# Kernel tuning notes

Hardware: AMD Instinct MI355X
Metric: run time of the kernel (lower is better)

Reference implementation:

```python
import jax, jax.numpy as jnp
import numpy as np

K, D = 4096, 256
BETA, DECAY, EPS = 0.25, 0.99, 1e-05
B = 32768


def setup_inputs() -> dict:
    key = jax.random.key(0)
    k1, k2, k3, k4 = jax.random.split(key, 4)
    return {
        "z_e": jax.random.normal(k1, (B, D), dtype=jnp.float32),
        "codebook": jax.random.normal(k2, (K, D), dtype=jnp.float32),
        "ema_cluster_size": jax.random.uniform(k3, (K,), dtype=jnp.float32),
        "ema_weight": jax.random.normal(k4, (K, D), dtype=jnp.float32),
    }


def reference(z_e, codebook, ema_cluster_size, ema_weight):
    z_e = z_e.astype(jnp.float32)
    # squared L2 distances: ||z||^2 - 2 z.C^T + ||C||^2  (chunking in torch is
    # purely a memory optimization; math is identical)
    e_norm = jnp.sum(z_e * z_e, axis=1, keepdims=True)            # [B,1]
    c_norm = jnp.sum(codebook * codebook, axis=1)                  # [K]
    dists = e_norm - 2.0 * (z_e @ codebook.T) + c_norm[None, :]    # [B,K]
    idx = jnp.argmin(dists, axis=1)                                # [B] int

    z_q = codebook[idx]                                            # [B,d] gather

    # EMA codebook update (no_grad in torch)
    counts = jnp.zeros((K,), jnp.float32).at[idx].add(1.0)         # bincount
    new_cluster = ema_cluster_size * DECAY + counts * (1.0 - DECAY)
    dw = jnp.zeros((K, D), jnp.float32).at[idx].add(z_e)           # index_add_
    new_ema_weight = ema_weight * DECAY + dw * (1.0 - DECAY)
    n = jnp.sum(new_cluster)
    cluster_size = (new_cluster + EPS) / (n + K * EPS) * n
    new_codebook = new_ema_weight / cluster_size[:, None]

    z_q_ste = z_e + jax.lax.stop_gradient(z_q - z_e)
    commit = BETA * jnp.mean((z_e - z_q) ** 2)
    return (z_q_ste, idx, commit, new_codebook, new_cluster, new_ema_weight)
```

## Files before the change

### kernel.cpp

```cpp
#include <hip/hip_runtime.h>

#define KC 4096
#define DD 256
#define BB 32768
#define P_BETA 0.25f
#define P_DECAY 0.99f
#define P_EPS 1e-5f
#define TAU 0.5f
#define CHUNK 32

typedef __attribute__((ext_vector_type(8))) short bf16x8;
typedef __attribute__((ext_vector_type(4))) float f32x4;

static __device__ __forceinline__ unsigned short f2bf(float f) {
    unsigned int u = __float_as_uint(f);
    unsigned int r = (u + 0x7fffu + ((u >> 16) & 1u)) >> 16;
    return (unsigned short)r;
}
static __device__ __forceinline__ void gload_lds16(const void* g, void* s) {
    __builtin_amdgcn_global_load_lds(
        (const __attribute__((address_space(1))) unsigned int*)g,
        (__attribute__((address_space(3))) unsigned int*)s, 16, 0, 0);
}

__global__ __launch_bounds__(256) void convert_z_kernel(const float* __restrict__ src,
                                                        unsigned short* __restrict__ dst) {
    int t = blockIdx.x * 256 + threadIdx.x;
    float4 v = ((const float4*)src)[t];
    *(ushort4*)&dst[(size_t)t * 4] =
        make_ushort4(f2bf(v.x), f2bf(v.y), f2bf(v.z), f2bf(v.w));
}

__global__ __launch_bounds__(256) void convert_cb_kernel(const float* __restrict__ cb,
                                                         unsigned short* __restrict__ dst,
                                                         float* __restrict__ cn) {
    int t = blockIdx.x * 256 + threadIdx.x;
    int lane = threadIdx.x & 63;
    int row = blockIdx.x * 4 + (threadIdx.x >> 6);
    float4 v = ((const float4*)cb)[t];
    *(ushort4*)&dst[(size_t)t * 4] =
        make_ushort4(f2bf(v.x), f2bf(v.y), f2bf(v.z), f2bf(v.w));
    float s = v.x * v.x + v.y * v.y + v.z * v.z + v.w * v.w;
#pragma unroll
    for (int m = 32; m; m >>= 1) s += __shfl_xor(s, m);
    if (lane == 0) cn[row] = s;
}

__global__ __launch_bounds__(256, 2) void
mfma_argmin_kernel(const unsigned short* __restrict__ zb,
                   const unsigned short* __restrict__ cbb,
                   const float* __restrict__ cn,
                   float4* __restrict__ cand) {
    __shared__ unsigned short As[128 * 256];
    __shared__ unsigned short Bs[128 * 64];

    const int tid = threadIdx.x;
    const int l = tid & 63, w = tid >> 6;
    const int xcd = blockIdx.x & 7;
    const int half = xcd >> 2;
    const int rb = (blockIdx.x >> 3) * 4 + (xcd & 3);
    const int row0 = rb * 128;
    const int col0 = half * 2048;
    const int wm = w & 1, wn = w >> 1;
    const int m_off = wm * 64, n_off = wn * 64;
    const int lm = l & 15, lq = l >> 4;

    {
        const int lrow = w * 2 + (l >> 5);
        const int coff = ((l & 31) ^ lrow) * 8;
#pragma unroll
        for (int i = 0; i < 16; ++i) {
            gload_lds16(zb + (size_t)(row0 + i * 8 + lrow) * DD + coff,
                        &As[(i * 8 + w * 2) * 256]);
        }
    }

    const int srow = l >> 3;
    const int scol = ((l & 7) ^ srow) * 8;
    const int g0 = w * 4;

    float best[16];
    int bidx[16];
#pragma unroll
    for (int s = 0; s < 16; ++s) { best[s] = 3.4e38f; bidx[s] = 0; }

    for (int kc = 0; kc < 2048; kc += 128) {
        f32x4 acc[4][4];
#pragma unroll
        for (int a = 0; a < 4; ++a)
#pragma unroll
            for (int b = 0; b < 4; ++b) acc[a][b] = (f32x4){0.f, 0.f, 0.f, 0.f};

        for (int dc = 0; dc < 4; ++dc) {
#pragma unroll
            for (int j = 0; j < 4; ++j) {
                const int g = g0 + j;
                const int br = col0 + kc + g * 8 + srow;
                gload_lds16(cbb + (size_t)br * DD + dc * 64 + scol, &Bs[g * 512]);
            }
            __syncthreads();
#pragma unroll
            for (int ks = 0; ks < 2; ++ks) {
                bf16x8 af[4], bfr[4];
                const int cbi = dc * 8 + ks * 4 + lq;
#pragma unroll
                for (int tm = 0; tm < 4; ++tm) {
                    int r = m_off + tm * 16 + lm;
                    af[tm] = *(const bf16x8*)&As[r * 256 + ((cbi ^ (r & 7)) * 8)];
                }
#pragma unroll
                for (int tn = 0; tn < 4; ++tn) {
                    int r = n_off + tn * 16 + lm;
                    bfr[tn] = *(const bf16x8*)&Bs[r * 64 + (((ks * 4 + lq) ^ (r & 7)) * 8)];
                }
#pragma unroll
                for (int tm = 0; tm < 4; ++tm)
#pragma unroll
                    for (int tn = 0; tn < 4; ++tn)
                        acc[tm][tn] = __builtin_amdgcn_mfma_f32_16x16x32_bf16(
                            af[tm], bfr[tn], acc[tm][tn], 0, 0, 0);
            }
            __syncthreads();
        }
#pragma unroll
        for (int tn = 0; tn < 4; ++tn) {
            const int col = col0 + kc + n_off + tn * 16 + lm;
            const float cnv = cn[col];
#pragma unroll
            for (int tm = 0; tm < 4; ++tm)
#pragma unroll
                for (int r = 0; r < 4; ++r) {
                    float dist = fmaf(-2.0f, acc[tm][tn][r], cnv);
                    int s = tm * 4 + r;
                    if (dist < best[s]) { best[s] = dist; bidx[s] = col; }
                }
        }
    }

    float v2[16];
    int i2[16];
#pragma unroll
    for (int s = 0; s < 16; ++s) { v2[s] = 3.4e38f; i2[s] = 0x7fffffff; }
#pragma unroll
    for (int m = 1; m < 16; m <<= 1) {
#pragma unroll
        for (int s = 0; s < 16; ++s) {
            float w1 = __shfl_xor(best[s], m); int j1 = __shfl_xor(bidx[s], m);
            float w2 = __shfl_xor(v2[s], m);   int j2 = __shfl_xor(i2[s], m);
            bool b = (w1 < best[s]) || (w1 == best[s] && j1 < bidx[s]);
            if (b) {
                bool c = (best[s] < w2) || (best[s] == w2 && bidx[s] < j2);
                v2[s] = c ? best[s] : w2; i2[s] = c ? bidx[s] : j2;
                best[s] = w1; bidx[s] = j1;
            } else {
                bool c = (w1 < v2[s]) || (w1 == v2[s] && j1 < i2[s]);
                v2[s] = c ? w1 : v2[s]; i2[s] = c ? j1 : i2[s];
            }
        }
    }

    float4* red = (float4*)As;
    if (lm == 0) {
#pragma unroll
        for (int tm = 0; tm < 4; ++tm)
#pragma unroll
            for (int r = 0; r < 4; ++r) {
                int s = tm * 4 + r;
                int row_local = m_off + tm * 16 + lq * 4 + r;
                red[wn * 128 + row_local] =
                    make_float4(best[s], __int_as_float(bidx[s]), v2[s], __int_as_float(i2[s]));
            }
    }
    __syncthreads();
    if (tid < 128) {
        float4 a = red[tid], b = red[128 + tid];
        float av1 = a.x, av2 = a.z; int ai1 = __float_as_int(a.y), ai2 = __float_as_int(a.w);
        float bv1 = b.x, bv2 = b.z; int bi1 = __float_as_int(b.y), bi2 = __float_as_int(b.w);
        float v1o, v2o; int i1o, i2o;
        bool bb = (bv1 < av1) || (bv1 == av1 && bi1 < ai1);
        if (bb) {
            v1o = bv1; i1o = bi1;
            bool c = (av1 < bv2) || (av1 == bv2 && ai1 < bi2);
            v2o = c ? av1 : bv2; i2o = c ? ai1 : bi2;
        } else {
            v1o = av1; i1o = ai1;
            bool c = (bv1 < av2) || (bv1 == av2 && bi1 < ai2);
            v2o = c ? bv1 : av2; i2o = c ? bi1 : ai2;
        }
        cand[(size_t)half * BB + row0 + tid] =
            make_float4(v1o, __int_as_float(i1o), v2o, __int_as_float(i2o));
    }
}

__global__ __launch_bounds__(256) void merge_kernel(
    const float4* __restrict__ cand, int* __restrict__ idx_i,
    float* __restrict__ idx_f, int4* __restrict__ wl, int* __restrict__ wl_cnt) {
    int i = blockIdx.x * 256 + threadIdx.x;
    float4 a = cand[i], b = cand[(size_t)BB + i];
    float av1 = a.x, av2 = a.z; int ai1 = __float_as_int(a.y), ai2 = __float_as_int(a.w);
    float bv1 = b.x, bv2 = b.z; int bi1 = __float_as_int(b.y), bi2 = __float_as_int(b.w);
    float v1o, v2o; int i1o, i2o;
    bool bb = (bv1 < av1) || (bv1 == av1 && bi1 < ai1);
    if (bb) {
        v1o = bv1; i1o = bi1;
        bool c = (av1 < bv2) || (av1 == bv2 && ai1 < bi2);
        v2o = c ? av1 : bv2; i2o = c ? ai1 : bi2;
    } else {
        v1o = av1; i1o = ai1;
        bool c = (bv1 < av2) || (bv1 == av2 && bi1 < ai2);
        v2o = c ? bv1 : av2; i2o = c ? bi1 : ai2;
    }
    idx_i[i] = i1o;
    idx_f[i] = (float)i1o;
    if (v2o - v1o < TAU) {
        int pos = atomicAdd(wl_cnt, 1);
        wl[pos] = make_int4(i, i1o, i2o, 0);
    }
}

__global__ __launch_bounds__(256) void refine_kernel(
    const int4* __restrict__ wl, const int* __restrict__ wl_cnt,
    const float* __restrict__ z, const float* __restrict__ cb,
    const float* __restrict__ cn, int* __restrict__ idx_i,
    float* __restrict__ idx_f) {
    const int wave = (blockIdx.x * 256 + threadIdx.x) >> 6;
    const int l = threadIdx.x & 63;
    const int n = *wl_cnt;
    for (int it = wave; it < n; it += 1024) {
        int4 e = wl[it];
        int i = e.x, k1 = e.y, k2 = e.z;
        float4 zv = ((const float4*)(z + (size_t)i * DD))[l];
        float4 p = ((const float4*)(cb + (size_t)k1 * DD))[l];
        float4 q = ((const float4*)(cb + (size_t)k2 * DD))[l];
        float s1 = zv.x * p.x + zv.y * p.y + zv.z * p.z + zv.w * p.w;
        float s2 = zv.x * q.x + zv.y * q.y + zv.z * q.z + zv.w * q.w;
#pragma unroll
        for (int m = 32; m; m >>= 1) { s1 += __shfl_xor(s1, m); s2 += __shfl_xor(s2, m); }
        float d1 = cn[k1] - 2.f * s1;
        float d2 = cn[k2] - 2.f * s2;
        int kb = (d2 < d1 || (d2 == d1 && k2 < k1)) ? k2 : k1;
        if (l == 0) { idx_i[i] = kb; idx_f[i] = (float)kb; }
    }
}

__global__ __launch_bounds__(256) void hist_kernel(const int* __restrict__ idx_i,
                                                   int* __restrict__ cnt) {
    int i = blockIdx.x * 256 + threadIdx.x;
    atomicAdd(&cnt[idx_i[i]], 1);
}

__global__ __launch_bounds__(256) void prefix_kernel(const int* __restrict__ cnt,
                                                     int* __restrict__ cursor) {
    __shared__ int ls[257];
    const int t = threadIdx.x;
    int local[16];
    int s = 0;
#pragma unroll
    for (int j = 0; j < 16; ++j) { local[j] = s; s += cnt[t * 16 + j]; }
    ls[t + 1] = s;
    __syncthreads();
    if (t == 0) {
        ls[0] = 0;
        for (int j = 1; j <= 256; ++j) ls[j] += ls[j - 1];
    }
    __syncthreads();
    int off = ls[t];
#pragma unroll
    for (int j = 0; j < 16; ++j) cursor[t * 16 + j] = off + local[j];
}

__global__ __launch_bounds__(256) void scatter_ids_kernel(const int* __restrict__ idx_i,
                                                          int* __restrict__ cursor,
                                                          int* __restrict__ row_of) {
    int i = blockIdx.x * 256 + threadIdx.x;
    int k = idx_i[i];
    int pos = atomicAdd(&cursor[k], 1);
    row_of[pos] = i | (k << 16);
}

__global__ __launch_bounds__(256) void bucket_chunk_kernel(
    const float* __restrict__ z, const int* __restrict__ row_of,
    float* __restrict__ dw) {
    __shared__ int pk[CHUNK];
    const int t = threadIdx.x;
    const int p0 = blockIdx.x * CHUNK;
    if (t < CHUNK) pk[t] = row_of[p0 + t];
    __syncthreads();
    float acc = 0.f;
    int kprev = pk[0] >> 16;
#pragma unroll 4
    for (int j = 0; j < CHUNK; ++j) {
        int p = pk[j];
        int r = p & 0xffff, k = p >> 16;
        if (k != kprev) {
            atomicAdd(&dw[(size_t)kprev * DD + t], acc);
            acc = 0.f;
            kprev = k;
        }
        acc += z[(size_t)r * DD + t];
    }
    atomicAdd(&dw[(size_t)kprev * DD + t], acc);
}

__global__ __launch_bounds__(256) void zq_commit_kernel(const float* __restrict__ z,
                                                        const float* __restrict__ cb,
                                                        const int* __restrict__ idx_i,
                                                        float* __restrict__ zq,
                                                        float* __restrict__ commit_parts) {
    const int w = threadIdx.x >> 6, l = threadIdx.x & 63;
    const int i = blockIdx.x * 4 + w;
    const int k = idx_i[i];
    float4 zv = ((const float4*)z)[(size_t)i * 64 + l];
    float4 cv = ((const float4*)cb)[(size_t)k * 64 + l];
    ((float4*)zq)[(size_t)i * 64 + l] = cv;
    float dx = zv.x - cv.x, dy = zv.y - cv.y, dz = zv.z - cv.z, dq = zv.w - cv.w;
    float s = dx * dx + dy * dy + dz * dz + dq * dq;
#pragma unroll
    for (int m = 32; m; m >>= 1) s += __shfl_xor(s, m);
    __shared__ float ls[4];
    if (l == 0) ls[w] = s;
    __syncthreads();
    if (threadIdx.x == 0) commit_parts[blockIdx.x] = ls[0] + ls[1] + ls[2] + ls[3];
}

__global__ __launch_bounds__(256) void cluster_commit_kernel(
    const float* __restrict__ ema_cs, const int* __restrict__ cnt,
    const float* __restrict__ commit_parts, float* __restrict__ out_cluster,
    float* __restrict__ n_ws, float* __restrict__ out_commit) {
    const int t = threadIdx.x;
    float cs = 0.f;
    for (int j = t; j < BB / 4; j += 256) cs += commit_parts[j];
    float ns = 0.f;
    for (int j = t; j < KC; j += 256) {
        float nc = ema_cs[j] * P_DECAY + (float)cnt[j] * (1.0f - P_DECAY);
        out_cluster[j] = nc;
        ns += nc;
    }
#pragma unroll
    for (int m = 32; m; m >>= 1) { cs += __shfl_xor(cs, m); ns += __shfl_xor(ns, m); }
    __shared__ float lc[4], ln[4];
    if ((t & 63) == 0) { lc[t >> 6] = cs; ln[t >> 6] = ns; }
    __syncthreads();
    if (t == 0) {
        *out_commit = P_BETA * (lc[0] + lc[1] + lc[2] + lc[3]) / (float)((size_t)BB * DD);
        *n_ws = ln[0] + ln[1] + ln[2] + ln[3];
    }
}

__global__ __launch_bounds__(256) void finalize_kernel(const float* __restrict__ ema_w,
                                                       const float* __restrict__ dw,
                                                       const float* __restrict__ out_cluster,
                                                       const float* __restrict__ n_ws,
                                                       float* __restrict__ out_ema_w,
                                                       float* __restrict__ out_codebook) {
    const size_t id = (size_t)blockIdx.x * 256 + threadIdx.x;
    const int k = (int)(id >> 8);
    const float n = *n_ws;
    float nw = ema_w[id] * P_DECAY + dw[id] * (1.0f - P_DECAY);
    out_ema_w[id] = nw;
    float cl = out_cluster[k];
    float csz = (cl + P_EPS) / (n + (float)KC * P_EPS) * n;
    out_codebook[id] = nw / csz;
}

extern "C" void kernel_launch(void* const* d_in, const int* in_sizes, int n_in,
                              void* d_out, int out_size, void* d_ws, size_t ws_size,
                              hipStream_t stream) {
    const float* z      = (const float*)d_in[0];
    const float* cb     = (const float*)d_in[1];
    const float* ema_cs = (const float*)d_in[2];
    const float* ema_w  = (const float*)d_in[3];

    float4* cand = (float4*)d_ws;
    int4* wl = (int4*)(cand + 2 * (size_t)BB);
    unsigned short* zb = (unsigned short*)(wl + BB);
    unsigned short* cbb = zb + (size_t)BB * DD;
    float* dw = (float*)(cbb + (size_t)KC * DD);
    float* c_norm = dw + (size_t)KC * DD;
    int* idx_i = (int*)(c_norm + KC);
    int* cnt = idx_i + BB;
    int* wl_cnt = cnt + KC;
    int* cursor = wl_cnt + 1;
    int* row_of = cursor + KC;
    float* commit_parts = (float*)(row_of + BB);
    float* n_ws = commit_parts + BB / 4;

    float* out        = (float*)d_out;
    float* o_zq       = out;
    float* o_idx      = o_zq + (size_t)BB * DD;
    float* o_commit   = o_idx + BB;
    float* o_codebook = o_commit + 1;
    float* o_cluster  = o_codebook + (size_t)KC * DD;
    float* o_emaw     = o_cluster + KC;

    hipMemsetAsync(cnt, 0, (KC + 1) * sizeof(int), stream);
    hipMemsetAsync(dw, 0, (size_t)KC * DD * sizeof(float), stream);

    convert_z_kernel<<<(BB * DD / 4) / 256, 256, 0, stream>>>(z, zb);
    convert_cb_kernel<<<KC / 4, 256, 0, stream>>>(cb, cbb, c_norm);
    mfma_argmin_kernel<<<(BB / 128) * 2, 256, 0, stream>>>(zb, cbb, c_norm, cand);
    merge_kernel<<<BB / 256, 256, 0, stream>>>(cand, idx_i, o_idx, wl, wl_cnt);
    refine_kernel<<<256, 256, 0, stream>>>(wl, wl_cnt, z, cb, c_norm, idx_i, o_idx);
    hist_kernel<<<BB / 256, 256, 0, stream>>>(idx_i, cnt);
    prefix_kernel<<<1, 256, 0, stream>>>(cnt, cursor);
    scatter_ids_kernel<<<BB / 256, 256, 0, stream>>>(idx_i, cursor, row_of);
    bucket_chunk_kernel<<<BB / CHUNK, 256, 0, stream>>>(z, row_of, dw);
    zq_commit_kernel<<<BB / 4, 256, 0, stream>>>(z, cb, idx_i, o_zq, commit_parts);
    cluster_commit_kernel<<<1, 256, 0, stream>>>(ema_cs, cnt, commit_parts,
                                                 o_cluster, n_ws, o_commit);
    finalize_kernel<<<(KC * DD) / 256, 256, 0, stream>>>(ema_w, dw, o_cluster, n_ws,
                                                         o_emaw, o_codebook);
    (void)in_sizes; (void)n_in; (void)out_size; (void)ws_size;
}
```

Measured before the change: 270.2 us.

## Fuse pipeline kernels to cut launches and memsets

After: 237.9 us. 1.14x faster.

```diff
diff --git a/kernel.cpp b/kernel.cpp
--- a/kernel.cpp
+++ b/kernel.cpp
@@ -23,27 +23,35 @@
         (__attribute__((address_space(3))) unsigned int*)s, 16, 0, 0);
 }
 
-__global__ __launch_bounds__(256) void convert_z_kernel(const float* __restrict__ src,
-                                                        unsigned short* __restrict__ dst) {
-    int t = blockIdx.x * 256 + threadIdx.x;
-    float4 v = ((const float4*)src)[t];
-    *(ushort4*)&dst[(size_t)t * 4] =
-        make_ushort4(f2bf(v.x), f2bf(v.y), f2bf(v.z), f2bf(v.w));
-}
-
-__global__ __launch_bounds__(256) void convert_cb_kernel(const float* __restrict__ cb,
-                                                         unsigned short* __restrict__ dst,
-                                                         float* __restrict__ cn) {
-    int t = blockIdx.x * 256 + threadIdx.x;
-    int lane = threadIdx.x & 63;
-    int row = blockIdx.x * 4 + (threadIdx.x >> 6);
-    float4 v = ((const float4*)cb)[t];
-    *(ushort4*)&dst[(size_t)t * 4] =
-        make_ushort4(f2bf(v.x), f2bf(v.y), f2bf(v.z), f2bf(v.w));
-    float s = v.x * v.x + v.y * v.y + v.z * v.z + v.w * v.w;
-#pragma unroll
-    for (int m = 32; m; m >>= 1) s += __shfl_xor(s, m);
-    if (lane == 0) cn[row] = s;
+#define ZBLK (BB * DD / 4 / 256)
+#define CBLK (KC * DD / 4 / 256)
+__global__ __launch_bounds__(256) void convert_all_kernel(
+    const float* __restrict__ z, const float* __restrict__ cb,
+    unsigned short* __restrict__ zb, unsigned short* __restrict__ cbb,
+    float* __restrict__ cn, int* __restrict__ cnt) {
+    const int b = blockIdx.x;
+    if (b < ZBLK) {
+        int t = b * 256 + threadIdx.x;
+        float4 v = ((const float4*)z)[t];
+        *(ushort4*)&zb[(size_t)t * 4] =
+            make_ushort4(f2bf(v.x), f2bf(v.y), f2bf(v.z), f2bf(v.w));
+    } else if (b < ZBLK + CBLK) {
+        int t = (b - ZBLK) * 256 + threadIdx.x;
+        int lane = threadIdx.x & 63;
+        int row = (b - ZBLK) * 4 + (threadIdx.x >> 6);
+        float4 v = ((const float4*)cb)[t];
+        *(ushort4*)&cbb[(size_t)t * 4] =
+            make_ushort4(f2bf(v.x), f2bf(v.y), f2bf(v.z), f2bf(v.w));
+        float s = v.x * v.x + v.y * v.y + v.z * v.z + v.w * v.w;
+#pragma unroll
+        for (int m = 32; m; m >>= 1) s += __shfl_xor(s, m);
+        if (lane == 0) cn[row] = s;
+    } else {
+        int4* p = (int4*)cnt;
+        int4 zv = make_int4(0, 0, 0, 0);
+#pragma unroll
+        for (int j = 0; j < 4; ++j) p[threadIdx.x * 4 + j] = zv;
+    }
 }
 
 __global__ __launch_bounds__(256, 2) void
@@ -192,10 +200,19 @@
     }
 }
 
-__global__ __launch_bounds__(256) void merge_kernel(
-    const float4* __restrict__ cand, int* __restrict__ idx_i,
-    float* __restrict__ idx_f, int4* __restrict__ wl, int* __restrict__ wl_cnt) {
+__global__ __launch_bounds__(256) void merge_refine_kernel(
+    const float4* __restrict__ cand, const float* __restrict__ z,
+    const float* __restrict__ cb, const float* __restrict__ cn,
+    int* __restrict__ idx_i, float* __restrict__ idx_f,
+    int* __restrict__ cnt, float* __restrict__ dw) {
     int i = blockIdx.x * 256 + threadIdx.x;
+    {
+        float4 zv4 = make_float4(0.f, 0.f, 0.f, 0.f);
+        float4* dp = (float4*)dw;
+        int base = i * 8;
+#pragma unroll
+        for (int j = 0; j < 8; ++j) dp[base + j] = zv4;
+    }
     float4 a = cand[i], b = cand[(size_t)BB + i];
     float av1 = a.x, av2 = a.z; int ai1 = __float_as_int(a.y), ai2 = __float_as_int(a.w);
     float bv1 = b.x, bv2 = b.z; int bi1 = __float_as_int(b.y), bi2 = __float_as_int(b.w);
@@ -210,43 +227,27 @@
         bool c = (bv1 < av2) || (bv1 == av2 && bi1 < ai2);
         v2o = c ? bv1 : av2; i2o = c ? bi1 : ai2;
     }
-    idx_i[i] = i1o;
-    idx_f[i] = (float)i1o;
+    int kb = i1o;
     if (v2o - v1o < TAU) {
-        int pos = atomicAdd(wl_cnt, 1);
-        wl[pos] = make_int4(i, i1o, i2o, 0);
-    }
-}
-
-__global__ __launch_bounds__(256) void refine_kernel(
-    const int4* __restrict__ wl, const int* __restrict__ wl_cnt,
-    const float* __restrict__ z, const float* __restrict__ cb,
-    const float* __restrict__ cn, int* __restrict__ idx_i,
-    float* __restrict__ idx_f) {
-    const int wave = (blockIdx.x * 256 + threadIdx.x) >> 6;
-    const int l = threadIdx.x & 63;
-    const int n = *wl_cnt;
-    for (int it = wave; it < n; it += 1024) {
-        int4 e = wl[it];
-        int i = e.x, k1 = e.y, k2 = e.z;
-        float4 zv = ((const float4*)(z + (size_t)i * DD))[l];
-        float4 p = ((const float4*)(cb + (size_t)k1 * DD))[l];
-        float4 q = ((const float4*)(cb + (size_t)k2 * DD))[l];
-        float s1 = zv.x * p.x + zv.y * p.y + zv.z * p.z + zv.w * p.w;
-        float s2 = zv.x * q.x + zv.y * q.y + zv.z * q.z + zv.w * q.w;
-#pragma unroll
-        for (int m = 32; m; m >>= 1) { s1 += __shfl_xor(s1, m); s2 += __shfl_xor(s2, m); }
-        float d1 = cn[k1] - 2.f * s1;
-        float d2 = cn[k2] - 2.f * s2;
-        int kb = (d2 < d1 || (d2 == d1 && k2 < k1)) ? k2 : k1;
-        if (l == 0) { idx_i[i] = kb; idx_f[i] = (float)kb; }
-    }
-}
-
-__global__ __launch_bounds__(256) void hist_kernel(const int* __restrict__ idx_i,
-                                                   int* __restrict__ cnt) {
-    int i = blockIdx.x * 256 + threadIdx.x;
-    atomicAdd(&cnt[idx_i[i]], 1);
+        const float4* zr = (const float4*)(z + (size_t)i * DD);
+        const float4* c1 = (const float4*)(cb + (size_t)i1o * DD);
+        const float4* c2 = (const float4*)(cb + (size_t)i2o * DD);
+        float s1x = 0, s1y = 0, s1z = 0, s1w = 0;
+        float s2x = 0, s2y = 0, s2z = 0, s2w = 0;
+        for (int j = 0; j < 64; ++j) {
+            float4 zv = zr[j], p = c1[j], q = c2[j];
+            s1x = fmaf(zv.x, p.x, s1x); s1y = fmaf(zv.y, p.y, s1y);
+            s1z = fmaf(zv.z, p.z, s1z); s1w = fmaf(zv.w, p.w, s1w);
+            s2x = fmaf(zv.x, q.x, s2x); s2y = fmaf(zv.y, q.y, s2y);
+            s2z = fmaf(zv.z, q.z, s2z); s2w = fmaf(zv.w, q.w, s2w);
+        }
+        float d1 = cn[i1o] - 2.f * ((s1x + s1y) + (s1z + s1w));
+        float d2 = cn[i2o] - 2.f * ((s2x + s2y) + (s2z + s2w));
+        if (d2 < d1 || (d2 == d1 && i2o < i1o)) kb = i2o;
+    }
+    idx_i[i] = kb;
+    idx_f[i] = (float)kb;
+    atomicAdd(&cnt[kb], 1);
 }
 
 __global__ __launch_bounds__(256) void prefix_kernel(const int* __restrict__ cnt,
@@ -269,20 +270,59 @@
     for (int j = 0; j < 16; ++j) cursor[t * 16 + j] = off + local[j];
 }
 
-__global__ __launch_bounds__(256) void scatter_ids_kernel(const int* __restrict__ idx_i,
-                                                          int* __restrict__ cursor,
-                                                          int* __restrict__ row_of) {
-    int i = blockIdx.x * 256 + threadIdx.x;
-    int k = idx_i[i];
-    int pos = atomicAdd(&cursor[k], 1);
-    row_of[pos] = i | (k << 16);
-}
-
-__global__ __launch_bounds__(256) void bucket_chunk_kernel(
+__global__ __launch_bounds__(256) void zq_commit_scatter_kernel(
+    const float* __restrict__ z, const float* __restrict__ cb,
+    const int* __restrict__ idx_i, float* __restrict__ zq,
+    float* __restrict__ commit_parts, int* __restrict__ cursor,
+    int* __restrict__ row_of) {
+    const int w = threadIdx.x >> 6, l = threadIdx.x & 63;
+    const int i = blockIdx.x * 4 + w;
+    const int k = idx_i[i];
+    float4 zv = ((const float4*)z)[(size_t)i * 64 + l];
+    float4 cv = ((const float4*)cb)[(size_t)k * 64 + l];
+    ((float4*)zq)[(size_t)i * 64 + l] = cv;
+    float dx = zv.x - cv.x, dy = zv.y - cv.y, dz = zv.z - cv.z, dq = zv.w - cv.w;
+    float s = dx * dx + dy * dy + dz * dz + dq * dq;
+#pragma unroll
+    for (int m = 32; m; m >>= 1) s += __shfl_xor(s, m);
+    __shared__ float ls[4];
+    if (l == 0) {
+        ls[w] = s;
+        int pos = atomicAdd(&cursor[k], 1);
+        row_of[pos] = i | (k << 16);
+    }
+    __syncthreads();
+    if (threadIdx.x == 0) commit_parts[blockIdx.x] = ls[0] + ls[1] + ls[2] + ls[3];
+}
+
+__global__ __launch_bounds__(256) void bucket_cluster_kernel(
     const float* __restrict__ z, const int* __restrict__ row_of,
-    float* __restrict__ dw) {
+    float* __restrict__ dw, const float* __restrict__ ema_cs,
+    const int* __restrict__ cnt, const float* __restrict__ commit_parts,
+    float* __restrict__ out_cluster, float* __restrict__ n_ws,
+    float* __restrict__ out_commit) {
+    const int t = threadIdx.x;
+    if (blockIdx.x == BB / CHUNK) {
+        float cs = 0.f;
+        for (int j = t; j < BB / 4; j += 256) cs += commit_parts[j];
+        float ns = 0.f;
+        for (int j = t; j < KC; j += 256) {
+            float nc = ema_cs[j] * P_DECAY + (float)cnt[j] * (1.0f - P_DECAY);
+            out_cluster[j] = nc;
+            ns += nc;
+        }
+#pragma unroll
+        for (int m = 32; m; m >>= 1) { cs += __shfl_xor(cs, m); ns += __shfl_xor(ns, m); }
+        __shared__ float lc[4], ln[4];
+        if ((t & 63) == 0) { lc[t >> 6] = cs; ln[t >> 6] = ns; }
+        __syncthreads();
+        if (t == 0) {
+            *out_commit = P_BETA * (lc[0] + lc[1] + lc[2] + lc[3]) / (float)((size_t)BB * DD);
+            *n_ws = ln[0] + ln[1] + ln[2] + ln[3];
+        }
+        return;
+    }
     __shared__ int pk[CHUNK];
-    const int t = threadIdx.x;
     const int p0 = blockIdx.x * CHUNK;
     if (t < CHUNK) pk[t] = row_of[p0 + t];
     __syncthreads();
@@ -300,51 +340,6 @@
         acc += z[(size_t)r * DD + t];
     }
     atomicAdd(&dw[(size_t)kprev * DD + t], acc);
-}
-
-__global__ __launch_bounds__(256) void zq_commit_kernel(const float* __restrict__ z,
-                                                        const float* __restrict__ cb,
-                                                        const int* __restrict__ idx_i,
-                                                        float* __restrict__ zq,
-                                                        float* __restrict__ commit_parts) {
-    const int w = threadIdx.x >> 6, l = threadIdx.x & 63;
-    const int i = blockIdx.x * 4 + w;
-    const int k = idx_i[i];
-    float4 zv = ((const float4*)z)[(size_t)i * 64 + l];
-    float4 cv = ((const float4*)cb)[(size_t)k * 64 + l];
-    ((float4*)zq)[(size_t)i * 64 + l] = cv;
-    float dx = zv.x - cv.x, dy = zv.y - cv.y, dz = zv.z - cv.z, dq = zv.w - cv.w;
-    float s = dx * dx + dy * dy + dz * dz + dq * dq;
-#pragma unroll
-    for (int m = 32; m; m >>= 1) s += __shfl_xor(s, m);
-    __shared__ float ls[4];
-    if (l == 0) ls[w] = s;
-    __syncthreads();
-    if (threadIdx.x == 0) commit_parts[blockIdx.x] = ls[0] + ls[1] + ls[2] + ls[3];
-}
-
-__global__ __launch_bounds__(256) void cluster_commit_kernel(
-    const float* __restrict__ ema_cs, const int* __restrict__ cnt,
-    const float* __restrict__ commit_parts, float* __restrict__ out_cluster,
-    float* __restrict__ n_ws, float* __restrict__ out_commit) {
-    const int t = threadIdx.x;
-    float cs = 0.f;
-    for (int j = t; j < BB / 4; j += 256) cs += commit_parts[j];
-    float ns = 0.f;
-    for (int j = t; j < KC; j += 256) {
-        float nc = ema_cs[j] * P_DECAY + (float)cnt[j] * (1.0f - P_DECAY);
-        out_cluster[j] = nc;
-        ns += nc;
-    }
-#pragma unroll
-    for (int m = 32; m; m >>= 1) { cs += __shfl_xor(cs, m); ns += __shfl_xor(ns, m); }
-    __shared__ float lc[4], ln[4];
-    if ((t & 63) == 0) { lc[t >> 6] = cs; ln[t >> 6] = ns; }
-    __syncthreads();
-    if (t == 0) {
-        *out_commit = P_BETA * (lc[0] + lc[1] + lc[2] + lc[3]) / (float)((size_t)BB * DD);
-        *n_ws = ln[0] + ln[1] + ln[2] + ln[3];
-    }
 }
 
 __global__ __launch_bounds__(256) void finalize_kernel(const float* __restrict__ ema_w,
@@ -372,15 +367,13 @@
     const float* ema_w  = (const float*)d_in[3];
 
     float4* cand = (float4*)d_ws;
-    int4* wl = (int4*)(cand + 2 * (size_t)BB);
-    unsigned short* zb = (unsigned short*)(wl + BB);
+    unsigned short* zb = (unsigned short*)(cand + 2 * (size_t)BB);
     unsigned short* cbb = zb + (size_t)BB * DD;
     float* dw = (float*)(cbb + (size_t)KC * DD);
     float* c_norm = dw + (size_t)KC * DD;
     int* idx_i = (int*)(c_norm + KC);
     int* cnt = idx_i + BB;
-    int* wl_cnt = cnt + KC;
-    int* cursor = wl_cnt + 1;
+    int* cursor = cnt + KC;
     int* row_of = cursor + KC;
     float* commit_parts = (float*)(row_of + BB);
     float* n_ws = commit_parts + BB / 4;
@@ -393,21 +386,16 @@
     float* o_cluster  = o_codebook + (size_t)KC * DD;
     float* o_emaw     = o_cluster + KC;
 
-    hipMemsetAsync(cnt, 0, (KC + 1) * sizeof(int), stream);
-    hipMemsetAsync(dw, 0, (size_t)KC * DD * sizeof(float), stream);
-
-    convert_z_kernel<<<(BB * DD / 4) / 256, 256, 0, stream>>>(z, zb);
-    convert_cb_kernel<<<KC / 4, 256, 0, stream>>>(cb, cbb, c_norm);
+    convert_all_kernel<<<ZBLK + CBLK + 1, 256, 0, stream>>>(z, cb, zb, cbb, c_norm, cnt);
     mfma_argmin_kernel<<<(BB / 128) * 2, 256, 0, stream>>>(zb, cbb, c_norm, cand);
-    merge_kernel<<<BB / 256, 256, 0, stream>>>(cand, idx_i, o_idx, wl, wl_cnt);
-    refine_kernel<<<256, 256, 0, stream>>>(wl, wl_cnt, z, cb, c_norm, idx_i, o_idx);
-    hist_kernel<<<BB / 256, 256, 0, stream>>>(idx_i, cnt);
+    merge_refine_kernel<<<BB / 256, 256, 0, stream>>>(cand, z, cb, c_norm, idx_i,
+                                                      o_idx, cnt, dw);
     prefix_kernel<<<1, 256, 0, stream>>>(cnt, cursor);
-    scatter_ids_kernel<<<BB / 256, 256, 0, stream>>>(idx_i, cursor, row_of);
-    bucket_chunk_kernel<<<BB / CHUNK, 256, 0, stream>>>(z, row_of, dw);
-    zq_commit_kernel<<<BB / 4, 256, 0, stream>>>(z, cb, idx_i, o_zq, commit_parts);
-    cluster_commit_kernel<<<1, 256, 0, stream>>>(ema_cs, cnt, commit_parts,
-                                                 o_cluster, n_ws, o_commit);
+    zq_commit_scatter_kernel<<<BB / 4, 256, 0, stream>>>(z, cb, idx_i, o_zq,
+                                                         commit_parts, cursor, row_of);
+    bucket_cluster_kernel<<<BB / CHUNK + 1, 256, 0, stream>>>(z, row_of, dw, ema_cs,
+                                                              cnt, commit_parts,
+                                                              o_cluster, n_ws, o_commit);
     finalize_kernel<<<(KC * DD) / 256, 256, 0, stream>>>(ema_w, dw, o_cluster, n_ws,
                                                          o_emaw, o_codebook);
     (void)in_sizes; (void)n_in; (void)out_size; (void)ws_size;
```
